# Performance work log

Measured on AMD Instinct MI355X. Metric: run time of the kernel, lower is better.

The kernel has to match this reference:

```python
import jax, jax.numpy as jnp
import numpy as np

T, H, I, E, TOPK = 1024, 1024, 2816, 16, 4


def setup_inputs() -> dict:
    key = jax.random.key(0)
    ks = jax.random.split(key, 5)
    s_h = 1.0 / np.sqrt(H)
    s_i = 1.0 / np.sqrt(I)
    return {
        "x": jax.random.normal(ks[0], (T, H), jnp.float32),
        "Wg": jax.random.normal(ks[1], (E, H), jnp.float32) * s_h,
        "gate_w": jax.random.normal(ks[2], (E, H, I), jnp.float32) * s_h,
        "up_w": jax.random.normal(ks[3], (E, H, I), jnp.float32) * s_h,
        "down_w": jax.random.normal(ks[4], (E, I, H), jnp.float32) * s_i,
        "top_k": TOPK,
    }


def reference(x, Wg, gate_w, up_w, down_w, top_k):
    # Router: softmax over expert logits, top-k, renormalize
    logits = x @ Wg.T                                   # [T, E]
    probs = jax.nn.softmax(logits, axis=-1)
    topk_w, topk_ids = jax.lax.top_k(probs, top_k)      # [T, K]
    topk_w = topk_w / jnp.sum(topk_w, axis=-1, keepdims=True)

    # Dense combine weights [T, E]: zero for unselected experts -> exact same
    # math as the per-token dispatch loop in the original module.
    n_tok = x.shape[0]
    combine = jnp.zeros((n_tok, Wg.shape[0]), x.dtype)
    combine = combine.at[jnp.arange(n_tok)[:, None], topk_ids].add(topk_w)

    # SwiGLU per expert, batched over the expert axis
    g = jax.nn.silu(jnp.einsum('th,ehi->eti', x, gate_w))  # [E, T, I]
    u = jnp.einsum('th,ehi->eti', x, up_w)                 # [E, T, I]
    y = jnp.einsum('eti,eih->eth', g * u, down_w)          # [E, T, H]

    # Weighted combine across experts
    return jnp.einsum('eth,te->th', y, combine)            # [T, H]
```

## Files before the change

### kernel.cpp

```cpp
#include <hip/hip_runtime.h>

static constexpr int cT = 1024;
static constexpr int cH = 1024;
static constexpr int cI = 2816;
static constexpr int cE = 16;
static constexpr int cK = 4;

typedef __attribute__((ext_vector_type(8))) short bf16x8;
typedef __attribute__((ext_vector_type(4))) float f32x4;
typedef __attribute__((ext_vector_type(2))) unsigned uint2v;
typedef __attribute__((ext_vector_type(4))) unsigned uint4v;

__device__ __forceinline__ unsigned f2bf(float f) {
  unsigned u = __float_as_uint(f);
  return (u + 0x7FFFu + ((u >> 16) & 1u)) >> 16;
}
__device__ __forceinline__ unsigned pack2(float lo, float hi) {
  return f2bf(lo) | (f2bf(hi) << 16);
}

__device__ __forceinline__ bf16x8 ld_bfrag(const unsigned* p) {
  union { uint2v d[2]; bf16x8 v; } r;
  r.d[0] = *(const uint2v*)p;
  r.d[1] = *(const uint2v*)(p + 2);
  return r.v;
}

__global__ __launch_bounds__(256) void xcast_kernel(
    const float* __restrict__ x, unsigned short* __restrict__ xb) {
  const int i = blockIdx.x * 256 + threadIdx.x;
  const float4* xv = (const float4*)x;
  const float4 a = xv[i * 2], b = xv[i * 2 + 1];
  uint4v o;
  o.x = pack2(a.x, a.y); o.y = pack2(a.z, a.w);
  o.z = pack2(b.x, b.y); o.w = pack2(b.z, b.w);
  ((uint4v*)xb)[i] = o;
}

__global__ __launch_bounds__(64) void router_kernel(
    const float* __restrict__ x, const float* __restrict__ Wg,
    int* __restrict__ topk_id, float* __restrict__ topk_w,
    int* __restrict__ counts) {
  const int t = blockIdx.x;
  const int l = threadIdx.x;

  float xa[16];
#pragma unroll
  for (int i = 0; i < 16; ++i) xa[i] = x[(size_t)t * cH + l + 64 * i];

  float lg[16];
#pragma unroll
  for (int e = 0; e < 16; ++e) {
    float s = 0.f;
#pragma unroll
    for (int i = 0; i < 16; ++i) s += xa[i] * Wg[(size_t)e * cH + l + 64 * i];
#pragma unroll
    for (int d = 1; d < 64; d <<= 1) s += __shfl_xor(s, d);
    lg[e] = s;
  }

  if (l == 0) {
    int ids[4]; float vals[4];
    unsigned taken = 0;
#pragma unroll
    for (int j = 0; j < 4; ++j) {
      float m = -1e30f; int mi = 0;
#pragma unroll
      for (int e = 0; e < 16; ++e) {
        bool better = !((taken >> e) & 1u) && lg[e] > m;
        if (better) { m = lg[e]; mi = e; }
      }
      taken |= 1u << mi; ids[j] = mi; vals[j] = m;
    }
    const float mx = vals[0];
    float s = 0.f;
#pragma unroll
    for (int j = 0; j < 4; ++j) { vals[j] = __expf(vals[j] - mx); s += vals[j]; }
    const float inv = 1.f / s;
#pragma unroll
    for (int j = 0; j < 4; ++j) {
      topk_id[t * 4 + j] = ids[j];
      topk_w[t * 4 + j] = vals[j] * inv;
      atomicAdd(&counts[ids[j]], 1);
    }
  }
}

__global__ void scan_kernel(const int* __restrict__ counts,
                            int* __restrict__ offsets) {
  if (threadIdx.x == 0 && blockIdx.x == 0) {
    int acc = 0;
    for (int e = 0; e < cE; ++e) { offsets[e] = acc; acc += counts[e]; }
    offsets[cE] = acc;
  }
}

__global__ __launch_bounds__(256) void scatter_kernel(
    const int* __restrict__ topk_id, const int* __restrict__ offsets,
    int* __restrict__ cursor, int* __restrict__ pair_token,
    int* __restrict__ pair_pos) {
  const int i = blockIdx.x * 256 + threadIdx.x;
  const int t = i >> 2;
  const int e = topk_id[i];
  const int pos = offsets[e] + atomicAdd(&cursor[e], 1);
  pair_token[pos] = t;
  pair_pos[i] = pos;
}

__global__ __launch_bounds__(256, 3) void gateup_kernel(
    const unsigned short* __restrict__ xb, const float* __restrict__ gw,
    const float* __restrict__ uw, const int* __restrict__ offsets,
    const int* __restrict__ pair_token, unsigned short* __restrict__ act) {
  const int e = blockIdx.y;
  const int off = offsets[e];
  const int n_e = offsets[e + 1] - off;
  const int strip = blockIdx.x / 3;
  const int c0 = (blockIdx.x % 3) * 128;
  if (c0 >= n_e) return;
  const int nb = strip * 64;
  const int tid = threadIdx.x, l = tid & 63, w = tid >> 6;

  __shared__ unsigned sB[2][2][2176];
  __shared__ int tokl[128];

  const int sa = tid >> 4;
  const int sc = tid & 15;
  const float* gb = gw + (size_t)e * cH * cI + nb + sc * 4;
  const float* ub = uw + (size_t)e * cH * cI + nb + sc * 4;

  for (int m0 = c0; m0 < n_e; m0 += 384) {
    if (tid < 128) tokl[tid] = pair_token[off + min(m0 + tid, n_e - 1)];
    __syncthreads();
    const int rows = min(128, n_e - m0);

    const unsigned short* ap[2];
#pragma unroll
    for (int mi = 0; mi < 2; ++mi) {
      const int idx = min(w * 32 + mi * 16 + (l & 15), rows - 1);
      ap[mi] = xb + (size_t)tokl[idx] * cH + (l >> 4) * 8;
    }

    f32x4 ag[2][4], au[2][4];
#pragma unroll
    for (int mi = 0; mi < 2; ++mi)
#pragma unroll
      for (int ni = 0; ni < 4; ++ni) {
        ag[mi][ni] = (f32x4){0.f, 0.f, 0.f, 0.f};
        au[mi][ni] = (f32x4){0.f, 0.f, 0.f, 0.f};
      }

    float4 rg[4], ru[4];
#pragma unroll
    for (int j = 0; j < 4; ++j) {
      rg[j] = *(const float4*)(gb + (size_t)(sa * 4 + j) * cI);
      ru[j] = *(const float4*)(ub + (size_t)(sa * 4 + j) * cI);
    }

    for (int kt = 0; kt < 16; ++kt) {
      const int cur = kt & 1;
      const int wbase = (sc * 4) * 34 + sa * 2;
#pragma unroll
      for (int i = 0; i < 4; ++i) {
        uint2v pg, pu;
        pg.x = pack2(rg[0][i], rg[1][i]); pg.y = pack2(rg[2][i], rg[3][i]);
        pu.x = pack2(ru[0][i], ru[1][i]); pu.y = pack2(ru[2][i], ru[3][i]);
        *(uint2v*)&sB[cur][0][wbase + i * 34] = pg;
        *(uint2v*)&sB[cur][1][wbase + i * 34] = pu;
      }
      if (kt + 1 < 16) {
#pragma unroll
        for (int j = 0; j < 4; ++j) {
          rg[j] = *(const float4*)(gb + (size_t)((kt + 1) * 64 + sa * 4 + j) * cI);
          ru[j] = *(const float4*)(ub + (size_t)((kt + 1) * 64 + sa * 4 + j) * cI);
        }
      }
      __syncthreads();

      bf16x8 av[2][2];
#pragma unroll
      for (int mi = 0; mi < 2; ++mi)
#pragma unroll
        for (int ks = 0; ks < 2; ++ks)
          av[mi][ks] = *(const bf16x8*)(ap[mi] + kt * 64 + ks * 32);

#pragma unroll
      for (int ks = 0; ks < 2; ++ks)
#pragma unroll
        for (int ni = 0; ni < 4; ++ni) {
          const int base = ((l & 15) + 16 * ni) * 34 + (l >> 4) * 4 + 16 * ks;
          const bf16x8 bg = ld_bfrag(&sB[cur][0][base]);
          const bf16x8 bu = ld_bfrag(&sB[cur][1][base]);
#pragma unroll
          for (int mi = 0; mi < 2; ++mi) {
            ag[mi][ni] = __builtin_amdgcn_mfma_f32_16x16x32_bf16(av[mi][ks], bg, ag[mi][ni], 0, 0, 0);
            au[mi][ni] = __builtin_amdgcn_mfma_f32_16x16x32_bf16(av[mi][ks], bu, au[mi][ni], 0, 0, 0);
          }
        }
    }

#pragma unroll
    for (int mi = 0; mi < 2; ++mi)
#pragma unroll
      for (int j = 0; j < 4; ++j) {
        const int er = m0 + w * 32 + mi * 16 + (l >> 4) * 4 + j;
        if (er < n_e) {
#pragma unroll
          for (int ni = 0; ni < 4; ++ni) {
            const float g = ag[mi][ni][j], u = au[mi][ni][j];
            const float v = (g / (1.f + __expf(-g))) * u;
            act[(size_t)(off + er) * cI + nb + ni * 16 + (l & 15)] =
                (unsigned short)f2bf(v);
          }
        }
      }
  }
}

__global__ __launch_bounds__(256, 4) void down_kernel(
    const unsigned short* __restrict__ act, const float* __restrict__ dw,
    const int* __restrict__ offsets, float* __restrict__ yp) {
  const int e = blockIdx.y;
  const int off = offsets[e];
  const int n_e = offsets[e + 1] - off;
  const int strip = blockIdx.x / 3;
  const int c0 = (blockIdx.x % 3) * 128;
  if (c0 >= n_e) return;
  const int nb = strip * 64;
  const int tid = threadIdx.x, l = tid & 63, w = tid >> 6;

  __shared__ unsigned sB[2][2176];

  const int sa = tid >> 4, sc = tid & 15;
  const float* db = dw + (size_t)e * cI * cH + nb + sc * 4;

  for (int m0 = c0; m0 < n_e; m0 += 384) {
    const int rows = min(128, n_e - m0);
    const unsigned short* ap[2];
#pragma unroll
    for (int mi = 0; mi < 2; ++mi) {
      const int r = min(m0 + w * 32 + mi * 16 + (l & 15), m0 + rows - 1);
      ap[mi] = act + (size_t)(off + r) * cI + (l >> 4) * 8;
    }

    f32x4 acc[2][4];
#pragma unroll
    for (int mi = 0; mi < 2; ++mi)
#pragma unroll
      for (int ni = 0; ni < 4; ++ni) acc[mi][ni] = (f32x4){0.f, 0.f, 0.f, 0.f};

    float4 rd[4];
#pragma unroll
    for (int j = 0; j < 4; ++j)
      rd[j] = *(const float4*)(db + (size_t)(sa * 4 + j) * cH);

    for (int kt = 0; kt < cI / 64; ++kt) {
      const int cur = kt & 1;
      const int wbase = (sc * 4) * 34 + sa * 2;
#pragma unroll
      for (int i = 0; i < 4; ++i) {
        uint2v p;
        p.x = pack2(rd[0][i], rd[1][i]); p.y = pack2(rd[2][i], rd[3][i]);
        *(uint2v*)&sB[cur][wbase + i * 34] = p;
      }
      if (kt + 1 < cI / 64) {
#pragma unroll
        for (int j = 0; j < 4; ++j)
          rd[j] = *(const float4*)(db + (size_t)((kt + 1) * 64 + sa * 4 + j) * cH);
      }
      __syncthreads();

      bf16x8 av[2][2];
#pragma unroll
      for (int mi = 0; mi < 2; ++mi)
#pragma unroll
        for (int ks = 0; ks < 2; ++ks)
          av[mi][ks] = *(const bf16x8*)(ap[mi] + kt * 64 + ks * 32);

#pragma unroll
      for (int ks = 0; ks < 2; ++ks)
#pragma unroll
        for (int ni = 0; ni < 4; ++ni) {
          const int base = ((l & 15) + 16 * ni) * 34 + (l >> 4) * 4 + 16 * ks;
          const bf16x8 b = ld_bfrag(&sB[cur][base]);
#pragma unroll
          for (int mi = 0; mi < 2; ++mi)
            acc[mi][ni] = __builtin_amdgcn_mfma_f32_16x16x32_bf16(av[mi][ks], b, acc[mi][ni], 0, 0, 0);
        }
    }

#pragma unroll
    for (int mi = 0; mi < 2; ++mi)
#pragma unroll
      for (int j = 0; j < 4; ++j) {
        const int er = m0 + w * 32 + mi * 16 + (l >> 4) * 4 + j;
        if (er < n_e) {
#pragma unroll
          for (int ni = 0; ni < 4; ++ni)
            yp[(size_t)(off + er) * cH + nb + ni * 16 + (l & 15)] = acc[mi][ni][j];
        }
      }
  }
}

__global__ __launch_bounds__(256) void combine_kernel(
    const float* __restrict__ yp, const int* __restrict__ pair_pos,
    const float* __restrict__ topk_w, float* __restrict__ out) {
  const int t = blockIdx.x;
  const int cb = threadIdx.x * 4;
  float4 s = make_float4(0.f, 0.f, 0.f, 0.f);
#pragma unroll
  for (int j = 0; j < 4; ++j) {
    const int pos = pair_pos[t * 4 + j];
    const float wj = topk_w[t * 4 + j];
    const float4 v = *(const float4*)(yp + (size_t)pos * cH + cb);
    s.x += wj * v.x; s.y += wj * v.y; s.z += wj * v.z; s.w += wj * v.w;
  }
  *(float4*)(out + (size_t)t * cH + cb) = s;
}

extern "C" void kernel_launch(void* const* d_in, const int* in_sizes, int n_in,
                              void* d_out, int out_size, void* d_ws,
                              size_t ws_size, hipStream_t stream) {
  (void)in_sizes; (void)n_in; (void)out_size; (void)ws_size;
  const float* x = (const float*)d_in[0];
  const float* Wg = (const float*)d_in[1];
  const float* gw = (const float*)d_in[2];
  const float* uw = (const float*)d_in[3];
  const float* dw = (const float*)d_in[4];
  float* out = (float*)d_out;

  char* ws = (char*)d_ws;
  int* counts     = (int*)(ws + 0);
  int* cursor     = (int*)(ws + 64);
  int* offsets    = (int*)(ws + 128);
  int* topk_id    = (int*)(ws + 256);
  float* topk_w   = (float*)(ws + 256 + 16384);
  int* pair_token = (int*)(ws + 256 + 32768);
  int* pair_pos   = (int*)(ws + 256 + 49152);
  unsigned short* act = (unsigned short*)(ws + 65792);
  unsigned short* xb  = (unsigned short*)(ws + 65792 + (size_t)4096 * 2816 * 2);
  float* yp = (float*)(ws + 65792 + (size_t)4096 * 2816 * 2 + (size_t)cT * cH * 2);

  hipMemsetAsync(ws, 0, 128, stream);

  xcast_kernel<<<cT * cH / (256 * 8), 256, 0, stream>>>(x, xb);
  router_kernel<<<cT, 64, 0, stream>>>(x, Wg, topk_id, topk_w, counts);
  scan_kernel<<<1, 1, 0, stream>>>(counts, offsets);
  scatter_kernel<<<cT * cK / 256, 256, 0, stream>>>(topk_id, offsets, cursor,
                                                    pair_token, pair_pos);
  gateup_kernel<<<dim3(44 * 3, cE), 256, 0, stream>>>(xb, gw, uw, offsets,
                                                      pair_token, act);
  down_kernel<<<dim3(16 * 3, cE), 256, 0, stream>>>(act, dw, offsets, yp);
  combine_kernel<<<cT, 256, 0, stream>>>(yp, pair_pos, topk_w, out);
}
```

Baseline: 408.8 us.

## Deepen weight prefetch, swizzle LDS tiles, and tile activation layout for down GEMM

Both expert GEMM kernels now prefetch weights two k-tiles ahead with ping-pong register sets, and the loop is unrolled by two. The tile is repacked into LDS with a 36-word row stride and an XOR-style swizzle so B fragments come out as single 128-bit reads. The gate/up kernel now splits the gate and up matrices across the two halves of the block. The intermediate activation is written in a blocked layout of 16 rows by 8 columns, so the down kernel's A-fragment loads are contiguous 16-byte chunks. This targets global-load latency, LDS bank conflicts and uncoalesced activation reads, at the cost of more registers and more complex indexing.

```diff
diff --git a/kernel.cpp b/kernel.cpp
--- a/kernel.cpp
+++ b/kernel.cpp
@@ -17,13 +17,6 @@
 }
 __device__ __forceinline__ unsigned pack2(float lo, float hi) {
   return f2bf(lo) | (f2bf(hi) << 16);
-}
-
-__device__ __forceinline__ bf16x8 ld_bfrag(const unsigned* p) {
-  union { uint2v d[2]; bf16x8 v; } r;
-  r.d[0] = *(const uint2v*)p;
-  r.d[1] = *(const uint2v*)(p + 2);
-  return r.v;
 }
 
 __global__ __launch_bounds__(256) void xcast_kernel(
@@ -107,10 +100,11 @@
   pair_pos[i] = pos;
 }
 
+
 __global__ __launch_bounds__(256, 3) void gateup_kernel(
     const unsigned short* __restrict__ xb, const float* __restrict__ gw,
     const float* __restrict__ uw, const int* __restrict__ offsets,
-    const int* __restrict__ pair_token, unsigned short* __restrict__ act) {
+    const int* __restrict__ pair_token, unsigned short* __restrict__ actT) {
   const int e = blockIdx.y;
   const int off = offsets[e];
   const int n_e = offsets[e + 1] - off;
@@ -119,105 +113,106 @@
   if (c0 >= n_e) return;
   const int nb = strip * 64;
   const int tid = threadIdx.x, l = tid & 63, w = tid >> 6;
-
-  __shared__ unsigned sB[2][2][2176];
+  const int q = l & 15, h16 = l >> 4;
+  const int hrd = 2 * ((q >> 2) & 3);
+
+  __shared__ unsigned sB[2][2][2304];
   __shared__ int tokl[128];
 
-  const int sa = tid >> 4;
-  const int sc = tid & 15;
-  const float* gb = gw + (size_t)e * cH * cI + nb + sc * 4;
-  const float* ub = uw + (size_t)e * cH * cI + nb + sc * 4;
+  const int mat = tid >> 7, tt = tid & 127, rg = tt >> 4, cg = tt & 15;
+  const int hwr = 2 * (cg & 3);
+  const float* wsrc = (mat ? uw : gw) + (size_t)e * cH * cI + nb + cg * 4;
+
+#define GU_LDSET(S, KT)                                                       \
+  _Pragma("unroll")                                                           \
+  for (int j = 0; j < 8; ++j)                                                 \
+    S[j] = *(const float4*)(wsrc + (size_t)((KT) * 64 + rg * 8 + j) * cI);
+
+#define GU_PACK(BUF, S)                                                       \
+  _Pragma("unroll")                                                           \
+  for (int i = 0; i < 4; ++i) {                                               \
+    uint4v P;                                                                 \
+    P.x = pack2(S[0][i], S[1][i]); P.y = pack2(S[2][i], S[3][i]);             \
+    P.z = pack2(S[4][i], S[5][i]); P.w = pack2(S[6][i], S[7][i]);             \
+    *(uint4v*)&sB[BUF][mat][(4 * cg + i) * 36 + 4 * ((rg + hwr) & 7)] = P;    \
+  }
+
+#define GU_TILE(KT, CUR, SC, SN)                                              \
+  {                                                                           \
+    if ((KT) + 2 < 16) { GU_LDSET(SC, (KT) + 2) }                             \
+    _Pragma("unroll")                                                         \
+    for (int ks = 0; ks < 2; ++ks) {                                          \
+      const bf16x8 a0 = *(const bf16x8*)(ap0 + (KT) * 64 + ks * 32);          \
+      const bf16x8 a1 = *(const bf16x8*)(ap1 + (KT) * 64 + ks * 32);          \
+      _Pragma("unroll")                                                       \
+      for (int ni = 0; ni < 4; ++ni) {                                        \
+        const int ba = (q + 16 * ni) * 36 + 4 * ((h16 + 4 * ks + hrd) & 7);   \
+        const bf16x8 bg = *(const bf16x8*)&sB[CUR][0][ba];                    \
+        const bf16x8 bu = *(const bf16x8*)&sB[CUR][1][ba];                    \
+        ag0[ni] = __builtin_amdgcn_mfma_f32_16x16x32_bf16(a0, bg, ag0[ni], 0, 0, 0); \
+        ag1[ni] = __builtin_amdgcn_mfma_f32_16x16x32_bf16(a1, bg, ag1[ni], 0, 0, 0); \
+        au0[ni] = __builtin_amdgcn_mfma_f32_16x16x32_bf16(a0, bu, au0[ni], 0, 0, 0); \
+        au1[ni] = __builtin_amdgcn_mfma_f32_16x16x32_bf16(a1, bu, au1[ni], 0, 0, 0); \
+      }                                                                       \
+    }                                                                         \
+    if ((KT) + 1 < 16) { GU_PACK(1 - (CUR), SN) __syncthreads(); }            \
+  }
 
   for (int m0 = c0; m0 < n_e; m0 += 384) {
     if (tid < 128) tokl[tid] = pair_token[off + min(m0 + tid, n_e - 1)];
     __syncthreads();
     const int rows = min(128, n_e - m0);
 
-    const unsigned short* ap[2];
-#pragma unroll
-    for (int mi = 0; mi < 2; ++mi) {
-      const int idx = min(w * 32 + mi * 16 + (l & 15), rows - 1);
-      ap[mi] = xb + (size_t)tokl[idx] * cH + (l >> 4) * 8;
-    }
-
-    f32x4 ag[2][4], au[2][4];
-#pragma unroll
-    for (int mi = 0; mi < 2; ++mi)
-#pragma unroll
-      for (int ni = 0; ni < 4; ++ni) {
-        ag[mi][ni] = (f32x4){0.f, 0.f, 0.f, 0.f};
-        au[mi][ni] = (f32x4){0.f, 0.f, 0.f, 0.f};
-      }
-
-    float4 rg[4], ru[4];
-#pragma unroll
-    for (int j = 0; j < 4; ++j) {
-      rg[j] = *(const float4*)(gb + (size_t)(sa * 4 + j) * cI);
-      ru[j] = *(const float4*)(ub + (size_t)(sa * 4 + j) * cI);
-    }
-
-    for (int kt = 0; kt < 16; ++kt) {
-      const int cur = kt & 1;
-      const int wbase = (sc * 4) * 34 + sa * 2;
-#pragma unroll
-      for (int i = 0; i < 4; ++i) {
-        uint2v pg, pu;
-        pg.x = pack2(rg[0][i], rg[1][i]); pg.y = pack2(rg[2][i], rg[3][i]);
-        pu.x = pack2(ru[0][i], ru[1][i]); pu.y = pack2(ru[2][i], ru[3][i]);
-        *(uint2v*)&sB[cur][0][wbase + i * 34] = pg;
-        *(uint2v*)&sB[cur][1][wbase + i * 34] = pu;
-      }
-      if (kt + 1 < 16) {
-#pragma unroll
-        for (int j = 0; j < 4; ++j) {
-          rg[j] = *(const float4*)(gb + (size_t)((kt + 1) * 64 + sa * 4 + j) * cI);
-          ru[j] = *(const float4*)(ub + (size_t)((kt + 1) * 64 + sa * 4 + j) * cI);
-        }
-      }
-      __syncthreads();
-
-      bf16x8 av[2][2];
-#pragma unroll
-      for (int mi = 0; mi < 2; ++mi)
-#pragma unroll
-        for (int ks = 0; ks < 2; ++ks)
-          av[mi][ks] = *(const bf16x8*)(ap[mi] + kt * 64 + ks * 32);
-
-#pragma unroll
-      for (int ks = 0; ks < 2; ++ks)
-#pragma unroll
-        for (int ni = 0; ni < 4; ++ni) {
-          const int base = ((l & 15) + 16 * ni) * 34 + (l >> 4) * 4 + 16 * ks;
-          const bf16x8 bg = ld_bfrag(&sB[cur][0][base]);
-          const bf16x8 bu = ld_bfrag(&sB[cur][1][base]);
-#pragma unroll
-          for (int mi = 0; mi < 2; ++mi) {
-            ag[mi][ni] = __builtin_amdgcn_mfma_f32_16x16x32_bf16(av[mi][ks], bg, ag[mi][ni], 0, 0, 0);
-            au[mi][ni] = __builtin_amdgcn_mfma_f32_16x16x32_bf16(av[mi][ks], bu, au[mi][ni], 0, 0, 0);
-          }
-        }
-    }
-
-#pragma unroll
-    for (int mi = 0; mi < 2; ++mi)
-#pragma unroll
-      for (int j = 0; j < 4; ++j) {
-        const int er = m0 + w * 32 + mi * 16 + (l >> 4) * 4 + j;
-        if (er < n_e) {
-#pragma unroll
-          for (int ni = 0; ni < 4; ++ni) {
-            const float g = ag[mi][ni][j], u = au[mi][ni][j];
-            const float v = (g / (1.f + __expf(-g))) * u;
-            act[(size_t)(off + er) * cI + nb + ni * 16 + (l & 15)] =
-                (unsigned short)f2bf(v);
-          }
-        }
-      }
-  }
+    const unsigned short* ap0 =
+        xb + (size_t)tokl[min(w * 32 + q, rows - 1)] * cH + h16 * 8;
+    const unsigned short* ap1 =
+        xb + (size_t)tokl[min(w * 32 + 16 + q, rows - 1)] * cH + h16 * 8;
+
+    f32x4 ag0[4], ag1[4], au0[4], au1[4];
+#pragma unroll
+    for (int ni = 0; ni < 4; ++ni) {
+      ag0[ni] = (f32x4){0.f, 0.f, 0.f, 0.f}; ag1[ni] = (f32x4){0.f, 0.f, 0.f, 0.f};
+      au0[ni] = (f32x4){0.f, 0.f, 0.f, 0.f}; au1[ni] = (f32x4){0.f, 0.f, 0.f, 0.f};
+    }
+
+    float4 s0[8], s1[8];
+    GU_LDSET(s0, 0)
+    GU_LDSET(s1, 1)
+    GU_PACK(0, s0)
+    __syncthreads();
+
+    for (int kt = 0; kt < 16; kt += 2) {
+      GU_TILE(kt, 0, s0, s1)
+      GU_TILE(kt + 1, 1, s1, s0)
+    }
+
+#define GU_EPI(MI, AGV, AUV)                                                  \
+  _Pragma("unroll")                                                           \
+  for (int j = 0; j < 4; ++j) {                                               \
+    const int er = m0 + w * 32 + (MI) * 16 + h16 * 4 + j;                     \
+    if (er < n_e) {                                                           \
+      const int p = off + er;                                                 \
+      const size_t pb = (size_t)(p >> 4) * 45056 + (p & 15) * 8 +             \
+                        (size_t)(nb >> 3) * 128 + (q & 7);                    \
+      _Pragma("unroll")                                                       \
+      for (int ni = 0; ni < 4; ++ni) {                                        \
+        const float g = AGV[ni][j], u = AUV[ni][j];                           \
+        const float v = (g / (1.f + __expf(-g))) * u;                         \
+        actT[pb + (size_t)(ni * 2 + (q >> 3)) * 128] = (unsigned short)f2bf(v); \
+      }                                                                       \
+    }                                                                         \
+  }
+    GU_EPI(0, ag0, au0)
+    GU_EPI(1, ag1, au1)
+  }
+#undef GU_LDSET
+#undef GU_PACK
+#undef GU_TILE
+#undef GU_EPI
 }
 
 __global__ __launch_bounds__(256, 4) void down_kernel(
-    const unsigned short* __restrict__ act, const float* __restrict__ dw,
+    const unsigned short* __restrict__ actT, const float* __restrict__ dw,
     const int* __restrict__ offsets, float* __restrict__ yp) {
   const int e = blockIdx.y;
   const int off = offsets[e];
@@ -227,79 +222,94 @@
   if (c0 >= n_e) return;
   const int nb = strip * 64;
   const int tid = threadIdx.x, l = tid & 63, w = tid >> 6;
-
-  __shared__ unsigned sB[2][2176];
-
-  const int sa = tid >> 4, sc = tid & 15;
-  const float* db = dw + (size_t)e * cI * cH + nb + sc * 4;
+  const int q = l & 15, h16 = l >> 4;
+  const int hrd = 2 * ((q >> 2) & 3);
+  constexpr int NT = cI / 64;
+
+  __shared__ unsigned sB[2][2304];
+
+  const int rg = tid >> 5, cg = (tid >> 1) & 15, half = tid & 1;
+  const int hwr = 2 * (cg & 3);
+  const float* dsrc = dw + (size_t)e * cI * cH + nb + cg * 4 + half * 2;
+
+#define DN_LDSET(S, KT)                                                       \
+  _Pragma("unroll")                                                           \
+  for (int j = 0; j < 8; ++j)                                                 \
+    S[j] = *(const float2*)(dsrc + (size_t)((KT) * 64 + rg * 8 + j) * cH);
+
+#define DN_PACK(BUF, S)                                                       \
+  _Pragma("unroll")                                                           \
+  for (int i = 0; i < 2; ++i) {                                               \
+    uint4v P;                                                                 \
+    const float* Sf = (const float*)S;                                        \
+    P.x = pack2(Sf[0 * 2 + i], Sf[1 * 2 + i]);                                \
+    P.y = pack2(Sf[2 * 2 + i], Sf[3 * 2 + i]);                                \
+    P.z = pack2(Sf[4 * 2 + i], Sf[5 * 2 + i]);                                \
+    P.w = pack2(Sf[6 * 2 + i], Sf[7 * 2 + i]);                                \
+    *(uint4v*)&sB[BUF][(4 * cg + 2 * half + i) * 36 + 4 * ((rg + hwr) & 7)] = P; \
+  }
+
+#define DN_TILE(KT, CUR, SC, SN)                                              \
+  {                                                                           \
+    if ((KT) + 2 < NT) { DN_LDSET(SC, (KT) + 2) }                             \
+    _Pragma("unroll")                                                         \
+    for (int ks = 0; ks < 2; ++ks) {                                          \
+      const bf16x8 a0 = *(const bf16x8*)(actT + b0 + (size_t)((KT) * 8 + h16 + 4 * ks) * 128); \
+      const bf16x8 a1 = *(const bf16x8*)(actT + b1 + (size_t)((KT) * 8 + h16 + 4 * ks) * 128); \
+      _Pragma("unroll")                                                       \
+      for (int ni = 0; ni < 4; ++ni) {                                        \
+        const int ba = (q + 16 * ni) * 36 + 4 * ((h16 + 4 * ks + hrd) & 7);   \
+        const bf16x8 b = *(const bf16x8*)&sB[CUR][ba];                        \
+        ac0[ni] = __builtin_amdgcn_mfma_f32_16x16x32_bf16(a0, b, ac0[ni], 0, 0, 0); \
+        ac1[ni] = __builtin_amdgcn_mfma_f32_16x16x32_bf16(a1, b, ac1[ni], 0, 0, 0); \
+      }                                                                       \
+    }                                                                         \
+    if ((KT) + 1 < NT) { DN_PACK(1 - (CUR), SN) __syncthreads(); }            \
+  }
 
   for (int m0 = c0; m0 < n_e; m0 += 384) {
-    const int rows = min(128, n_e - m0);
-    const unsigned short* ap[2];
-#pragma unroll
-    for (int mi = 0; mi < 2; ++mi) {
-      const int r = min(m0 + w * 32 + mi * 16 + (l & 15), m0 + rows - 1);
-      ap[mi] = act + (size_t)(off + r) * cI + (l >> 4) * 8;
-    }
-
-    f32x4 acc[2][4];
-#pragma unroll
-    for (int mi = 0; mi < 2; ++mi)
-#pragma unroll
-      for (int ni = 0; ni < 4; ++ni) acc[mi][ni] = (f32x4){0.f, 0.f, 0.f, 0.f};
-
-    float4 rd[4];
-#pragma unroll
-    for (int j = 0; j < 4; ++j)
-      rd[j] = *(const float4*)(db + (size_t)(sa * 4 + j) * cH);
-
-    for (int kt = 0; kt < cI / 64; ++kt) {
-      const int cur = kt & 1;
-      const int wbase = (sc * 4) * 34 + sa * 2;
-#pragma unroll
-      for (int i = 0; i < 4; ++i) {
-        uint2v p;
-        p.x = pack2(rd[0][i], rd[1][i]); p.y = pack2(rd[2][i], rd[3][i]);
-        *(uint2v*)&sB[cur][wbase + i * 34] = p;
-      }
-      if (kt + 1 < cI / 64) {
-#pragma unroll
-        for (int j = 0; j < 4; ++j)
-          rd[j] = *(const float4*)(db + (size_t)((kt + 1) * 64 + sa * 4 + j) * cH);
-      }
-      __syncthreads();
-
-      bf16x8 av[2][2];
-#pragma unroll
-      for (int mi = 0; mi < 2; ++mi)
-#pragma unroll
-        for (int ks = 0; ks < 2; ++ks)
-          av[mi][ks] = *(const bf16x8*)(ap[mi] + kt * 64 + ks * 32);
-
-#pragma unroll
-      for (int ks = 0; ks < 2; ++ks)
-#pragma unroll
-        for (int ni = 0; ni < 4; ++ni) {
-          const int base = ((l & 15) + 16 * ni) * 34 + (l >> 4) * 4 + 16 * ks;
-          const bf16x8 b = ld_bfrag(&sB[cur][base]);
-#pragma unroll
-          for (int mi = 0; mi < 2; ++mi)
-            acc[mi][ni] = __builtin_amdgcn_mfma_f32_16x16x32_bf16(av[mi][ks], b, acc[mi][ni], 0, 0, 0);
-        }
-    }
-
-#pragma unroll
-    for (int mi = 0; mi < 2; ++mi)
-#pragma unroll
-      for (int j = 0; j < 4; ++j) {
-        const int er = m0 + w * 32 + mi * 16 + (l >> 4) * 4 + j;
-        if (er < n_e) {
-#pragma unroll
-          for (int ni = 0; ni < 4; ++ni)
-            yp[(size_t)(off + er) * cH + nb + ni * 16 + (l & 15)] = acc[mi][ni][j];
-        }
-      }
-  }
+    const int p0g = off + min(m0 + w * 32 + q, n_e - 1);
+    const int p1g = off + min(m0 + w * 32 + 16 + q, n_e - 1);
+    const size_t b0 = (size_t)(p0g >> 4) * 45056 + (p0g & 15) * 8;
+    const size_t b1 = (size_t)(p1g >> 4) * 45056 + (p1g & 15) * 8;
+
+    f32x4 ac0[4], ac1[4];
+#pragma unroll
+    for (int ni = 0; ni < 4; ++ni) {
+      ac0[ni] = (f32x4){0.f, 0.f, 0.f, 0.f};
+      ac1[ni] = (f32x4){0.f, 0.f, 0.f, 0.f};
+    }
+
+    float2 s0[8], s1[8];
+    DN_LDSET(s0, 0)
+    DN_LDSET(s1, 1)
+    DN_PACK(0, s0)
+    __syncthreads();
+
+    for (int kt = 0; kt < NT; kt += 2) {
+      DN_TILE(kt, 0, s0, s1)
+      DN_TILE(kt + 1, 1, s1, s0)
+    }
+
+#define DN_EPI(MI, ACV)                                                       \
+  _Pragma("unroll")                                                           \
+  for (int j = 0; j < 4; ++j) {                                               \
+    const int er = m0 + w * 32 + (MI) * 16 + h16 * 4 + j;                     \
+    if (er < n_e) {                                                           \
+      _Pragma("unroll")                                                       \
+      for (int ni = 0; ni < 4; ++ni)                                          \
+        yp[(size_t)(off + er) * cH + nb + ni * 16 + q] = ACV[ni][j];          \
+    }                                                                         \
+  }
+    DN_EPI(0, ac0)
+    DN_EPI(1, ac1)
+
+    if (m0 + 384 < n_e) __syncthreads();
+  }
+#undef DN_LDSET
+#undef DN_PACK
+#undef DN_TILE
+#undef DN_EPI
 }
 
 __global__ __launch_bounds__(256) void combine_kernel(
@@ -337,8 +347,8 @@
   float* topk_w   = (float*)(ws + 256 + 16384);
   int* pair_token = (int*)(ws + 256 + 32768);
   int* pair_pos   = (int*)(ws + 256 + 49152);
-  unsigned short* act = (unsigned short*)(ws + 65792);
-  unsigned short* xb  = (unsigned short*)(ws + 65792 + (size_t)4096 * 2816 * 2);
+  unsigned short* actT = (unsigned short*)(ws + 65792);
+  unsigned short* xb   = (unsigned short*)(ws + 65792 + (size_t)4096 * 2816 * 2);
   float* yp = (float*)(ws + 65792 + (size_t)4096 * 2816 * 2 + (size_t)cT * cH * 2);
 
   hipMemsetAsync(ws, 0, 128, stream);
@@ -349,7 +359,7 @@
   scatter_kernel<<<cT * cK / 256, 256, 0, stream>>>(topk_id, offsets, cursor,
                                                     pair_token, pair_pos);
   gateup_kernel<<<dim3(44 * 3, cE), 256, 0, stream>>>(xb, gw, uw, offsets,
-                                                      pair_token, act);
-  down_kernel<<<dim3(16 * 3, cE), 256, 0, stream>>>(act, dw, offsets, yp);
+                                                      pair_token, actT);
+  down_kernel<<<dim3(16 * 3, cE), 256, 0, stream>>>(actT, dw, offsets, yp);
   combine_kernel<<<cT, 256, 0, stream>>>(yp, pair_pos, topk_w, out);
 }
```

Result: slower. 491.1 us (+20.1%).
